# Kernel optimization log

Measured on AMD Instinct MI355X. Metric: run time of the kernel, lower is better.

Reference implementation:

```python
import jax, jax.numpy as jnp
import numpy as np

B, N, C, PH, PW = 16, 256, 1, 16, 16
G, HID = 8, 256
TEMP = 0.5
EPS = 1e-5


def setup_inputs() -> dict:
    key = jax.random.key(0)
    ks = jax.random.split(key, 16)
    f32 = jnp.float32
    def kaiming(k, shape):  # fan_out mode for convs, OIHW
        fan_out = shape[0] * shape[2] * shape[3]
        return jax.random.normal(k, shape, f32) * np.float32(np.sqrt(2.0 / fan_out))
    def lin(k, shape):  # nn.init.normal_(w, 0, 0.01)
        return jax.random.normal(k, shape, f32) * np.float32(0.01)
    return {
        "x": jax.random.normal(ks[0], (B, N, C, PH, PW), f32),
        "conv1_w": kaiming(ks[1], (32, 1, 3, 3)),  "conv1_b": jnp.zeros((32,), f32),
        "bn1_g": jnp.ones((32,), f32),  "bn1_b": jnp.zeros((32,), f32),
        "conv2_w": kaiming(ks[2], (64, 32, 3, 3)), "conv2_b": jnp.zeros((64,), f32),
        "bn2_g": jnp.ones((64,), f32),  "bn2_b": jnp.zeros((64,), f32),
        "conv3_w": kaiming(ks[3], (128, 64, 3, 3)), "conv3_b": jnp.zeros((128,), f32),
        "bn3_g": jnp.ones((128,), f32), "bn3_b": jnp.zeros((128,), f32),
        "fc_w": lin(ks[4], (HID, 128)),       "fc_b": jnp.zeros((HID,), f32),
        "g1_w": lin(ks[5], (2 * HID, HID)),   "g1_b": jnp.zeros((2 * HID,), f32),
        "ln1_g": jnp.ones((2 * HID,), f32),   "ln1_b": jnp.zeros((2 * HID,), f32),
        "g2_w": lin(ks[6], (2 * HID, 2 * HID)), "g2_b": jnp.zeros((2 * HID,), f32),
        "ln2_g": jnp.ones((2 * HID,), f32),   "ln2_b": jnp.zeros((2 * HID,), f32),
        "g3_w": lin(ks[7], (G, 2 * HID)),     "g3_b": jnp.zeros((G,), f32),
    }


def _conv(h, w, b):
    out = jax.lax.conv_general_dilated(h, w, (1, 1), 'SAME',
        dimension_numbers=('NCHW', 'OIHW', 'NCHW'))
    return out + b[None, :, None, None]


def _bn_train(h, g, b):  # batch stats over (N, H, W), biased variance
    m = h.mean(axis=(0, 2, 3), keepdims=True)
    v = h.var(axis=(0, 2, 3), keepdims=True)
    return (h - m) * jax.lax.rsqrt(v + EPS) * g[None, :, None, None] + b[None, :, None, None]


def _ln(h, g, b):
    m = h.mean(axis=-1, keepdims=True)
    v = h.var(axis=-1, keepdims=True)
    return (h - m) * jax.lax.rsqrt(v + EPS) * g + b


def reference(x, conv1_w, conv1_b, bn1_g, bn1_b, conv2_w, conv2_b, bn2_g, bn2_b,
              conv3_w, conv3_b, bn3_g, bn3_b, fc_w, fc_b,
              g1_w, g1_b, ln1_g, ln1_b, g2_w, g2_b, ln2_g, ln2_b, g3_w, g3_b):
    Bx, Nx, Cx, ph, pw = x.shape
    Gx = g3_w.shape[0]
    K = Nx // Gx  # num_patches_per_group

    # ---- patch encoder (conv + BN(train) + ReLU x3, GAP, Linear) ----
    h = x.reshape(Bx * Nx, Cx, ph, pw)
    h = jax.nn.relu(_bn_train(_conv(h, conv1_w, conv1_b), bn1_g, bn1_b))
    h = jax.nn.relu(_bn_train(_conv(h, conv2_w, conv2_b), bn2_g, bn2_b))
    h = jax.nn.relu(_bn_train(_conv(h, conv3_w, conv3_b), bn3_g, bn3_b))
    feat = h.mean(axis=(2, 3))                     # [B*N, 128] (AdaptiveAvgPool2d(1))
    feat = feat @ fc_w.T + fc_b                    # [B*N, HID]
    feat = feat.reshape(Bx, Nx, -1)

    # ---- grouping network ----
    h = jax.nn.relu(_ln(feat @ g1_w.T + g1_b, ln1_g, ln1_b))
    h = jax.nn.relu(_ln(h @ g2_w.T + g2_b, ln2_g, ln2_b))
    logits = (h @ g3_w.T + g3_b) / TEMP            # [B, N, G]
    assignment = jax.nn.softmax(logits, axis=2)    # [B, N, G]

    # ---- per-group top-K weighted patch gather (training path) ----
    w = jnp.transpose(assignment, (0, 2, 1))       # [B, G, N]
    vals, idx = jax.lax.top_k(w, K)                # [B, G, K] (descending, matches sort)
    idx_e = idx[:, :, :, None, None, None]         # [B, G, K, 1, 1, 1]
    gathered = jnp.take_along_axis(x[:, None], idx_e, axis=2)  # [B, G, K, C, ph, pw]
    output = gathered * vals[:, :, :, None, None, None]
    return output, assignment
```

## Files before the change

### kernel.cpp

```cpp
#include <hip/hip_runtime.h>


typedef float f32x16 __attribute__((ext_vector_type(16)));

#define WS_W1   0
#define WS_B1   288
#define WS_W2   320
#define WS_B2   18752
#define WS_W3   18816
#define WS_B3   92544
#define WS_FCW  92672
#define WS_FCB  125440
#define WS_G1W  125696
#define WS_G1B  256768
#define WS_L1G  257280
#define WS_L1B  257792
#define WS_G2W  258304
#define WS_G2B  520448
#define WS_L2G  520960
#define WS_L2B  521472
#define WS_G3W  521984
#define WS_G3B  526080
#define D_ACC1  263044
#define D_ACC2  (D_ACC1 + 4096)
#define D_ACC3  (D_ACC2 + 8192)
#define D_FEAT  (D_ACC3 + 16384)
#define D_AFF1  (D_FEAT + 524288)
#define D_AFF2  (D_AFF1 + 64)
#define D_AFF3  (D_AFF2 + 128)
#define D_ZN    553408
#define Z2_OFF_B 6532096ull


__global__ __launch_bounds__(256) void k_zero(double* __restrict__ dst){
  int i = blockIdx.x*256 + threadIdx.x;
  if(i < D_ZN) dst[i] = 0.0;
}

struct WP { const float* p[18]; };

__global__ __launch_bounds__(256) void k_cvt(WP wp, float* __restrict__ dst){
  const int segn[18] = {288,32,18432,64,73728,128,32768,256,131072,512,512,512,262144,512,512,512,4096,8};
  const int sego[18] = {WS_W1,WS_B1,WS_W2,WS_B2,WS_W3,WS_B3,WS_FCW,WS_FCB,WS_G1W,WS_G1B,
                        WS_L1G,WS_L1B,WS_G2W,WS_G2B,WS_L2G,WS_L2B,WS_G3W,WS_G3B};
  int s = blockIdx.y;
  int i = blockIdx.x*256 + threadIdx.x;
  if(i < segn[s]){
    if(s == 4){
      int oc = i / 576;
      int rem = i - oc*576;
      int ic = rem / 9;
      int j  = rem - ic*9;
      dst[WS_W3 + ic*1152 + j*128 + oc] = wp.p[4][i];
    } else {
      dst[sego[s]+i] = wp.p[s][i];
    }
  }
}

__global__ __launch_bounds__(64) void k_fin(const double* __restrict__ acc, int C,
                                            const float* __restrict__ gam, const float* __restrict__ bet,
                                            double* __restrict__ aff){
  int c = blockIdx.x, t = threadIdx.x;
  double s = acc[t*2*C + c*2];
  double q = acc[t*2*C + c*2 + 1];
  #pragma unroll
  for(int off=32;off;off>>=1){ s += __shfl_down(s,off); q += __shfl_down(q,off); }
  if(t==0){
    double m = s*(1.0/1048576.0);
    double v = q*(1.0/1048576.0) - m*m;
    double sc = (double)gam[c] / sqrt(v + 1e-5);
    aff[2*c]   = sc;
    aff[2*c+1] = (double)bet[c] - m*sc;
  }
}

__global__ __launch_bounds__(256) void k_p1(const float* __restrict__ x, const float* __restrict__ wf,
                                            double* __restrict__ acc1){
  __shared__ float xp[324];
  __shared__ double red[4][32][2];
  int p = blockIdx.x, t = threadIdx.x;
  for(int i=t;i<324;i+=256) xp[i]=0.f;
  __syncthreads();
  int py=t>>4, px=t&15;
  xp[(py+1)*18 + px + 1] = x[(size_t)p*256+t];
  __syncthreads();
  float nb[9];
  #pragma unroll
  for(int j=0;j<9;j++) nb[j] = xp[(py+j/3)*18 + px + (j%3)];
  int wave=t>>6, lane=t&63;
  for(int c=0;c<32;c++){
    float a = wf[WS_B1+c];
    #pragma unroll
    for(int j=0;j<9;j++) a = fmaf(nb[j], wf[WS_W1+c*9+j], a);
    double av=(double)a;
    double s=av, q=av*av;
    #pragma unroll
    for(int off=32;off;off>>=1){ s+=__shfl_down(s,off); q+=__shfl_down(q,off); }
    if(lane==0){ red[wave][c][0]=s; red[wave][c][1]=q; }
  }
  __syncthreads();
  if(t<64){
    int c=t>>1, st=t&1;
    double v = red[0][c][st]+red[1][c][st]+red[2][c][st]+red[3][c][st];
    atomicAdd(&acc1[(p&63)*64 + c*2 + st], v);
  }
}

__global__ __launch_bounds__(256) void k_p2(const float* __restrict__ x, const float* __restrict__ wf,
                                            const double* __restrict__ aff1, double* __restrict__ acc2,
                                            float* __restrict__ z2, int nS){
  __shared__ float xp[324];
  __shared__ float h1f[32*324];
  int p=blockIdx.x, t=threadIdx.x;
  for(int i=t;i<324;i+=256) xp[i]=0.f;
  for(int i=t;i<32*324;i+=256) h1f[i]=0.f;
  __syncthreads();
  int py=t>>4, px=t&15;
  xp[(py+1)*18 + px + 1] = x[(size_t)p*256+t];
  __syncthreads();
  {
    float nb[9];
    #pragma unroll
    for(int j=0;j<9;j++) nb[j] = xp[(py+j/3)*18 + px + (j%3)];
    for(int c=0;c<32;c++){
      float a = wf[WS_B1+c];
      #pragma unroll
      for(int j=0;j<9;j++) a = fmaf(nb[j], wf[WS_W1+c*9+j], a);
      h1f[c*324 + (py+1)*18 + (px+1)] = fmaxf(fmaf((float)aff1[2*c], a, (float)aff1[2*c+1]), 0.f);
    }
  }
  __syncthreads();
  int col=t&15, og=t>>4;
  bool wr = (p < nS);
  double sT[4]={0,0,0,0}, qT[4]={0,0,0,0};
  #pragma unroll 1
  for(int half=0; half<2; ++half){
    float acc[4][8];
    #pragma unroll
    for(int o=0;o<4;o++){
      float bv = wf[WS_B2 + og*4 + o];
      #pragma unroll
      for(int r=0;r<8;r++) acc[o][r]=bv;
    }
    #pragma unroll 1
    for(int ic=0; ic<32; ++ic){
      const float* wrow = wf + WS_W2 + (og*4*32 + ic)*9;
      #pragma unroll
      for(int j=0;j<9;j++){
        float w4[4];
        #pragma unroll
        for(int o=0;o<4;o++) w4[o] = wrow[o*288 + j];
        int dy=j/3, dx=j%3;
        #pragma unroll
        for(int r=0;r<8;r++){
          float m = h1f[ic*324 + (half*8 + r + dy)*18 + col + dx];
          #pragma unroll
          for(int o=0;o<4;o++) acc[o][r] = fmaf(m, w4[o], acc[o][r]);
        }
      }
    }
    #pragma unroll
    for(int o=0;o<4;o++){
      #pragma unroll
      for(int r=0;r<8;r++){ double v=(double)acc[o][r]; sT[o]+=v; qT[o]+=v*v; }
      if(wr){
        int c = og*4+o;
        #pragma unroll
        for(int r=0;r<8;r++) z2[((size_t)p*64+c)*256 + (half*8+r)*16 + col] = acc[o][r];
      }
    }
  }
  #pragma unroll
  for(int o=0;o<4;o++){
    double s=sT[o], q=qT[o];
    #pragma unroll
    for(int off=8;off;off>>=1){ s+=__shfl_down(s,off,16); q+=__shfl_down(q,off,16); }
    if(col==0){
      int c = og*4+o;
      atomicAdd(&acc2[(p&63)*128 + c*2 + 0], s);
      atomicAdd(&acc2[(p&63)*128 + c*2 + 1], q);
    }
  }
}

__global__ __launch_bounds__(512) void k_cs(const float* __restrict__ wf, const double* __restrict__ aff2,
                                            double* __restrict__ acc3, const float* __restrict__ z2){
  __shared__ float h2S[32*360];
  int p=blockIdx.x, t=threadIdx.x;
  for(int i=t;i<11520;i+=512) h2S[i]=0.f;
  int col=t&15, q=(t>>4)&3;
  int wv = __builtin_amdgcn_readfirstlane(t>>6);
  float acc[16][4];
  #pragma unroll
  for(int o=0;o<16;o++){
    float bv = wf[WS_B3 + wv*16 + o];
    #pragma unroll
    for(int r=0;r<4;r++) acc[o][r]=bv;
  }
  const f32x16* wW = reinterpret_cast<const f32x16*>(wf + WS_W3 + wv*16);
  #pragma unroll 1
  for(int half=0; half<2; ++half){
    __syncthreads();
    for(int i=t;i<8192;i+=512){
      int ch2 = i>>8, rem = i&255, gr = rem>>4, c2 = rem&15;
      int ch = half*32 + ch2;
      float zv = z2[((size_t)p*64+ch)*256 + gr*16 + c2];
      h2S[ch2*360 + (gr+1)*20 + c2+1] = fmaxf(fmaf((float)aff2[2*ch], zv, (float)aff2[2*ch+1]), 0.f);
    }
    __syncthreads();
    #pragma unroll 1
    for(int ic2=0; ic2<32; ++ic2){
      int ic = half*32 + ic2;
      float a[6][3];
      #pragma unroll
      for(int lr=0; lr<6; ++lr){
        #pragma unroll
        for(int dx=0; dx<3; ++dx) a[lr][dx] = h2S[ic2*360 + (4*q+lr)*20 + col + dx];
      }
      #pragma unroll
      for(int j=0;j<9;j++){
        f32x16 w = wW[ic*72 + j*8];
        int dy=j/3, dx=j%3;
        #pragma unroll
        for(int o=0;o<16;o++){
          #pragma unroll
          for(int r=0;r<4;r++) acc[o][r] = fmaf(a[r+dy][dx], w[o], acc[o][r]);
        }
      }
    }
  }
  #pragma unroll
  for(int o=0;o<16;o++){
    double s=0.0, q2=0.0;
    #pragma unroll
    for(int r=0;r<4;r++){ double v=(double)acc[o][r]; s+=v; q2+=v*v; }
    #pragma unroll
    for(int off=32;off;off>>=1){ s += __shfl_down(s,off); q2 += __shfl_down(q2,off); }
    if((t&63)==0){
      int c = wv*16+o;
      atomicAdd(&acc3[(p&63)*256 + c*2 + 0], s);
      atomicAdd(&acc3[(p&63)*256 + c*2 + 1], q2);
    }
  }
}

__global__ __launch_bounds__(512) void k_cf(const float* __restrict__ wf, const double* __restrict__ aff2,
                                            const double* __restrict__ aff3, double* __restrict__ feat,
                                            const float* __restrict__ z2){
  __shared__ float h2S[32*360];
  int p=blockIdx.x, t=threadIdx.x;
  for(int i=t;i<11520;i+=512) h2S[i]=0.f;
  int col=t&15, q=(t>>4)&3;
  int wv = __builtin_amdgcn_readfirstlane(t>>6);
  float acc[16][4];
  #pragma unroll
  for(int o=0;o<16;o++){
    float bv = wf[WS_B3 + wv*16 + o];
    #pragma unroll
    for(int r=0;r<4;r++) acc[o][r]=bv;
  }
  const f32x16* wW = reinterpret_cast<const f32x16*>(wf + WS_W3 + wv*16);
  #pragma unroll 1
  for(int half=0; half<2; ++half){
    __syncthreads();
    for(int i=t;i<8192;i+=512){
      int ch2 = i>>8, rem = i&255, gr = rem>>4, c2 = rem&15;
      int ch = half*32 + ch2;
      float zv = z2[((size_t)p*64+ch)*256 + gr*16 + c2];
      h2S[ch2*360 + (gr+1)*20 + c2+1] = fmaxf(fmaf((float)aff2[2*ch], zv, (float)aff2[2*ch+1]), 0.f);
    }
    __syncthreads();
    #pragma unroll 1
    for(int ic2=0; ic2<32; ++ic2){
      int ic = half*32 + ic2;
      float a[6][3];
      #pragma unroll
      for(int lr=0; lr<6; ++lr){
        #pragma unroll
        for(int dx=0; dx<3; ++dx) a[lr][dx] = h2S[ic2*360 + (4*q+lr)*20 + col + dx];
      }
      #pragma unroll
      for(int j=0;j<9;j++){
        f32x16 w = wW[ic*72 + j*8];
        int dy=j/3, dx=j%3;
        #pragma unroll
        for(int o=0;o<16;o++){
          #pragma unroll
          for(int r=0;r<4;r++) acc[o][r] = fmaf(a[r+dy][dx], w[o], acc[o][r]);
        }
      }
    }
  }
  #pragma unroll
  for(int o=0;o<16;o++){
    int c = wv*16+o;
    float sc=(float)aff3[2*c], sh=(float)aff3[2*c+1];
    double sv = 0.0;
    #pragma unroll
    for(int r=0;r<4;r++) sv += (double)fmaxf(fmaf(sc, acc[o][r], sh), 0.f);
    #pragma unroll
    for(int off=32;off;off>>=1) sv += __shfl_down(sv,off);
    if((t&63)==0) atomicAdd(&feat[(size_t)p*128 + c], sv);
  }
}

__global__ __launch_bounds__(256) void k_stat3(const float* __restrict__ x, const float* __restrict__ wf,
                                               const double* __restrict__ aff1, const double* __restrict__ aff2,
                                               double* __restrict__ acc3, int p0){
  __shared__ float xp[324];
  __shared__ float h1S[32*144];
  __shared__ float h2S[64*108];
  int bid=blockIdx.x, t=threadIdx.x;
  int p = p0 + (bid>>2), r0 = (bid&3)*4;
  for(int i=t;i<64*108;i+=256) h2S[i]=0.f;
  for(int i=t;i<324;i+=256) xp[i]=0.f;
  for(int i=t;i<32*144;i+=256) h1S[i]=0.f;
  __syncthreads();
  { int py=t>>4, px=t&15; xp[(py+1)*18 + px + 1] = x[(size_t)p*256+t]; }
  __syncthreads();
  {
    int rr=t>>5, cw=t&31, col=cw&15, half=cw>>4;
    int p1 = r0-1+rr;
    if(p1>=1 && p1<=16){
      float nb[9];
      #pragma unroll
      for(int j=0;j<9;j++) nb[j] = xp[(p1-1+j/3)*18 + col + (j%3)];
      for(int k=0;k<16;k++){
        int c = half*16+k;
        float a = wf[WS_B1+c];
        #pragma unroll
        for(int j=0;j<9;j++) a = fmaf(nb[j], wf[WS_W1+c*9+j], a);
        h1S[c*144 + rr*18 + col+1] = fmaxf((float)aff1[2*c]*a + (float)aff1[2*c+1], 0.f);
      }
    }
  }
  __syncthreads();
  {
    int col=t&15, g=t>>4;
    float a24[4][6];
    #pragma unroll
    for(int o=0;o<4;o++){
      float bv = wf[WS_B2+g*4+o];
      #pragma unroll
      for(int b2=0;b2<6;b2++) a24[o][b2] = bv;
    }
    #pragma unroll 1
    for(int ic=0;ic<32;ic++){
      const float* wrow = wf + WS_W2 + (g*4*32 + ic)*9;
      #pragma unroll
      for(int j=0;j<9;j++){
        float w4[4];
        #pragma unroll
        for(int o=0;o<4;o++) w4[o] = wrow[o*288 + j];
        int dy=j/3, dx=j%3;
        #pragma unroll
        for(int b2=0;b2<6;b2++){
          float m = h1S[ic*144 + (b2+dy)*18 + col + dx];
          #pragma unroll
          for(int o=0;o<4;o++) a24[o][b2] = fmaf(m, w4[o], a24[o][b2]);
        }
      }
    }
    #pragma unroll
    for(int b2=0;b2<6;b2++){
      int p2 = r0+b2;
      if(p2>=1 && p2<=16){
        #pragma unroll
        for(int o=0;o<4;o++){
          int c=g*4+o;
          h2S[c*108 + b2*18 + col+1] = fmaxf((float)aff2[2*c]*a24[o][b2] + (float)aff2[2*c+1], 0.f);
        }
      }
    }
  }
  __syncthreads();
  {
    int col = t & 15, og = t >> 4;
    float acc[8][4];
    #pragma unroll
    for(int o=0;o<8;o++){
      float bv = wf[WS_B3 + og*8 + o];
      #pragma unroll
      for(int r=0;r<4;r++) acc[o][r] = bv;
    }
    #pragma unroll 1
    for(int ic=0; ic<64; ++ic){
      float a[6][3];
      #pragma unroll
      for(int rr=0; rr<6; ++rr){
        #pragma unroll
        for(int dx=0; dx<3; ++dx) a[rr][dx] = h2S[ic*108 + rr*18 + col + dx];
      }
      const float* wrow = wf + WS_W3 + ic*1152;
      #pragma unroll
      for(int o=0;o<8;o++){
        #pragma unroll
        for(int j=0;j<9;j++){
          float w = wrow[j*128 + og*8 + o];
          #pragma unroll
          for(int r=0;r<4;r++) acc[o][r] = fmaf(a[r + j/3][j%3], w, acc[o][r]);
        }
      }
    }
    #pragma unroll
    for(int o=0;o<8;o++){
      double s=0.0, q=0.0;
      #pragma unroll
      for(int r=0;r<4;r++){ double v=(double)acc[o][r]; s+=v; q+=v*v; }
      #pragma unroll
      for(int off=8; off; off>>=1){ s += __shfl_down(s, off, 16); q += __shfl_down(q, off, 16); }
      if(col==0){
        int c = og*8+o;
        atomicAdd(&acc3[(bid&63)*256 + c*2 + 0], s);
        atomicAdd(&acc3[(bid&63)*256 + c*2 + 1], q);
      }
    }
  }
}

__global__ __launch_bounds__(256) void k_p34(const float* __restrict__ x, const float* __restrict__ wf,
                                             const double* __restrict__ aff1, const double* __restrict__ aff2,
                                             const double* __restrict__ aff3, double* __restrict__ outp,
                                             int p0){
  __shared__ float xp[324];
  __shared__ float h1S[32*144];
  __shared__ float h2S[64*108];
  int bid=blockIdx.x, t=threadIdx.x;
  int p = p0 + (bid>>2), r0 = (bid&3)*4;
  for(int i=t;i<64*108;i+=256) h2S[i]=0.f;
  for(int i=t;i<324;i+=256) xp[i]=0.f;
  for(int i=t;i<32*144;i+=256) h1S[i]=0.f;
  __syncthreads();
  { int py=t>>4, px=t&15; xp[(py+1)*18 + px + 1] = x[(size_t)p*256+t]; }
  __syncthreads();
  {
    int rr=t>>5, cw=t&31, col=cw&15, half=cw>>4;
    int p1 = r0-1+rr;
    if(p1>=1 && p1<=16){
      float nb[9];
      #pragma unroll
      for(int j=0;j<9;j++) nb[j] = xp[(p1-1+j/3)*18 + col + (j%3)];
      for(int k=0;k<16;k++){
        int c = half*16+k;
        float a = wf[WS_B1+c];
        #pragma unroll
        for(int j=0;j<9;j++) a = fmaf(nb[j], wf[WS_W1+c*9+j], a);
        h1S[c*144 + rr*18 + col+1] = fmaxf((float)aff1[2*c]*a + (float)aff1[2*c+1], 0.f);
      }
    }
  }
  __syncthreads();
  {
    int col=t&15, g=t>>4;
    float a24[4][6];
    #pragma unroll
    for(int o=0;o<4;o++){
      float bv = wf[WS_B2+g*4+o];
      #pragma unroll
      for(int b2=0;b2<6;b2++) a24[o][b2] = bv;
    }
    #pragma unroll 1
    for(int ic=0;ic<32;ic++){
      const float* wrow = wf + WS_W2 + (g*4*32 + ic)*9;
      #pragma unroll
      for(int j=0;j<9;j++){
        float w4[4];
        #pragma unroll
        for(int o=0;o<4;o++) w4[o] = wrow[o*288 + j];
        int dy=j/3, dx=j%3;
        #pragma unroll
        for(int b2=0;b2<6;b2++){
          float m = h1S[ic*144 + (b2+dy)*18 + col + dx];
          #pragma unroll
          for(int o=0;o<4;o++) a24[o][b2] = fmaf(m, w4[o], a24[o][b2]);
        }
      }
    }
    #pragma unroll
    for(int b2=0;b2<6;b2++){
      int p2 = r0+b2;
      if(p2>=1 && p2<=16){
        #pragma unroll
        for(int o=0;o<4;o++){
          int c=g*4+o;
          h2S[c*108 + b2*18 + col+1] = fmaxf((float)aff2[2*c]*a24[o][b2] + (float)aff2[2*c+1], 0.f);
        }
      }
    }
  }
  __syncthreads();
  {
    int col = t & 15, og = t >> 4;
    float acc[8][4];
    #pragma unroll
    for(int o=0;o<8;o++){
      float bv = wf[WS_B3 + og*8 + o];
      #pragma unroll
      for(int r=0;r<4;r++) acc[o][r] = bv;
    }
    #pragma unroll 1
    for(int ic=0; ic<64; ++ic){
      float a[6][3];
      #pragma unroll
      for(int rr=0; rr<6; ++rr){
        #pragma unroll
        for(int dx=0; dx<3; ++dx) a[rr][dx] = h2S[ic*108 + rr*18 + col + dx];
      }
      const float* wrow = wf + WS_W3 + ic*1152;
      #pragma unroll
      for(int o=0;o<8;o++){
        #pragma unroll
        for(int j=0;j<9;j++){
          float w = wrow[j*128 + og*8 + o];
          #pragma unroll
          for(int r=0;r<4;r++) acc[o][r] = fmaf(a[r + j/3][j%3], w, acc[o][r]);
        }
      }
    }
    #pragma unroll
    for(int o=0;o<8;o++){
      int c = og*8+o;
      float sc=(float)aff3[2*c], sh=(float)aff3[2*c+1];
      double s = 0.0;
      #pragma unroll
      for(int r=0;r<4;r++) s += (double)fmaxf(fmaf(sc, acc[o][r], sh), 0.f);
      #pragma unroll
      for(int off=8; off; off>>=1) s += __shfl_down(s, off, 16);
      if(col==0) atomicAdd(&outp[(size_t)p*128 + c], s);
    }
  }
}

__device__ __forceinline__ void ln_relu4(double* buf, const float* __restrict__ g, const float* __restrict__ b,
                                         double* lnm, double* lnr, int t){
  int r=t>>6, j=t&63;
  double s=0.0, q=0.0;
  for(int k=j;k<512;k+=64){ double v=buf[r*512+k]; s+=v; q+=v*v; }
  #pragma unroll
  for(int off=32;off;off>>=1){ s+=__shfl_down(s,off); q+=__shfl_down(q,off); }
  if(j==0){
    double m = s*(1.0/512.0);
    double v = q*(1.0/512.0) - m*m;
    lnm[r]=m; lnr[r]=1.0/sqrt(v + 1e-5);
  }
  __syncthreads();
  for(int i=t;i<2048;i+=256){
    int r2=i>>9, k=i&511;
    double v=(buf[i]-lnm[r2])*lnr[r2]*(double)g[k]+(double)b[k];
    buf[i]=fmax(v,0.0);
  }
  __syncthreads();
}

__global__ __launch_bounds__(256) void k_mlp(const float* __restrict__ wf, const double* __restrict__ feat,
                                             float* __restrict__ assign_out){
  int r0 = blockIdx.x*4, t = threadIdx.x;
  __shared__ double f0[4*128];
  __shared__ double f1[4*256];
  __shared__ double f2[4*512];
  __shared__ double f3[4*512];
  __shared__ double lnm[4], lnr[4];
  __shared__ double lg[4][8];

  for(int i=t;i<512;i+=256) f0[i] = feat[(size_t)r0*128 + i] * (1.0/256.0);
  __syncthreads();
  {
    double acc[4];
    double bv = (double)wf[WS_FCB + t];
    #pragma unroll
    for(int r=0;r<4;r++) acc[r]=bv;
    for(int k=0;k<128;k++){
      double wv = (double)wf[WS_FCW + t*128 + k];
      #pragma unroll
      for(int r=0;r<4;r++) acc[r]=fma(wv, f0[r*128+k], acc[r]);
    }
    #pragma unroll
    for(int r=0;r<4;r++) f1[r*256+t]=acc[r];
  }
  __syncthreads();
  for(int half=0;half<2;half++){
    int i=t+(half<<8);
    double acc[4];
    double bv=(double)wf[WS_G1B+i];
    #pragma unroll
    for(int r=0;r<4;r++) acc[r]=bv;
    for(int k=0;k<256;k++){
      double wv=(double)wf[WS_G1W + i*256 + k];
      #pragma unroll
      for(int r=0;r<4;r++) acc[r]=fma(wv, f1[r*256+k], acc[r]);
    }
    #pragma unroll
    for(int r=0;r<4;r++) f2[r*512+i]=acc[r];
  }
  __syncthreads();
  ln_relu4(f2, wf+WS_L1G, wf+WS_L1B, lnm, lnr, t);
  for(int half=0;half<2;half++){
    int i=t+(half<<8);
    double acc[4];
    double bv=(double)wf[WS_G2B+i];
    #pragma unroll
    for(int r=0;r<4;r++) acc[r]=bv;
    for(int k=0;k<512;k++){
      double wv=(double)wf[WS_G2W + i*512 + k];
      #pragma unroll
      for(int r=0;r<4;r++) acc[r]=fma(wv, f2[r*512+k], acc[r]);
    }
    #pragma unroll
    for(int r=0;r<4;r++) f3[r*512+i]=acc[r];
  }
  __syncthreads();
  ln_relu4(f3, wf+WS_L2G, wf+WS_L2B, lnm, lnr, t);
  {
    int r=t>>6, j=t&63;
    double pl[8];
    #pragma unroll
    for(int g=0;g<8;g++){
      double s=0.0;
      for(int k=j;k<512;k+=64) s = fma(f3[r*512+k], (double)wf[WS_G3W + g*512 + k], s);
      pl[g]=s;
    }
    #pragma unroll
    for(int off=32;off;off>>=1){
      #pragma unroll
      for(int g=0;g<8;g++) pl[g] += __shfl_down(pl[g], off);
    }
    if(j==0){
      #pragma unroll
      for(int g=0;g<8;g++) lg[r][g] = (pl[g] + (double)wf[WS_G3B+g]) * 2.0;
    }
  }
  __syncthreads();
  if(t<4){
    double m=-1e300;
    #pragma unroll
    for(int g=0;g<8;g++) m = fmax(m, lg[t][g]);
    double e[8], s=0.0;
    #pragma unroll
    for(int g=0;g<8;g++){ e[g]=exp(lg[t][g]-m); s+=e[g]; }
    double inv = 1.0/s;
    int row = r0 + t;
    #pragma unroll
    for(int g=0;g<8;g++) assign_out[row*8+g] = (float)(e[g]*inv);
  }
}

__global__ __launch_bounds__(256) void k_topk(const float* __restrict__ assign, const float* __restrict__ x,
                                              float* __restrict__ out){
  int b = blockIdx.x >> 3, g = blockIdx.x & 7, t = threadIdx.x;
  __shared__ float v[256];
  __shared__ int   id[256];
  v[t] = assign[(b*256+t)*8 + g];
  id[t] = t;
  __syncthreads();
  for(int k=2;k<=256;k<<=1){
    for(int j=k>>1;j>0;j>>=1){
      int ixj = t ^ j;
      if(ixj > t){
        float va=v[t], vb=v[ixj];
        int ia=id[t], ib=id[ixj];
        bool aBefore = (va > vb) || (va == vb && ia < ib);
        bool up = ((t & k) == 0);
        if(up != aBefore){ v[t]=vb; v[ixj]=va; id[t]=ib; id[ixj]=ia; }
      }
      __syncthreads();
    }
  }
  __shared__ float tv[32];
  __shared__ int   ti[32];
  if(t<32){ tv[t]=v[t]; ti[t]=id[t]; }
  __syncthreads();
  const float* xb = x + (size_t)b*65536;
  float* ob = out + (size_t)(b*8+g)*8192;
  for(int i=t;i<8192;i+=256){
    int k=i>>8, pix=i&255;
    ob[i] = tv[k] * xb[ti[k]*256 + pix];
  }
}

extern "C" void kernel_launch(void* const* d_in, const int* in_sizes, int n_in,
                              void* d_out, int out_size, void* d_ws, size_t ws_size,
                              hipStream_t stream){
  const float* x = (const float*)d_in[0];
  float*  ws  = (float*)d_ws;
  double* dws = (double*)d_ws;
  float* out = (float*)d_out;
  float* assign_out = out + 1048576;
  float* z2 = (float*)((char*)d_ws + Z2_OFF_B);

  int nS = 0;
  if(ws_size > Z2_OFF_B + 65536){
    unsigned long long avail = (unsigned long long)ws_size - Z2_OFF_B;
    unsigned long long n = avail / 65536ull;
    nS = (n > 4096ull) ? 4096 : (int)n;
  }
  int nR = 4096 - nS;

  const float* g1=(const float*)d_in[3];  const float* b1=(const float*)d_in[4];
  const float* g2=(const float*)d_in[7];  const float* b2=(const float*)d_in[8];
  const float* g3=(const float*)d_in[11]; const float* b3=(const float*)d_in[12];

  WP wp;
  const int map[18] = {1,2,5,6,9,10,13,14,15,16,17,18,19,20,21,22,23,24};
  for(int i=0;i<18;i++) wp.p[i] = (const float*)d_in[map[i]];

  k_zero <<<2162, 256, 0, stream>>>(dws + D_ACC1);
  k_cvt  <<<dim3(1024,18), 256, 0, stream>>>(wp, ws);
  k_p1   <<<4096, 256, 0, stream>>>(x, ws, dws+D_ACC1);
  k_fin  <<<32, 64, 0, stream>>>(dws+D_ACC1, 32, g1, b1, dws+D_AFF1);
  k_p2   <<<4096, 256, 0, stream>>>(x, ws, dws+D_AFF1, dws+D_ACC2, z2, nS);
  k_fin  <<<64, 64, 0, stream>>>(dws+D_ACC2, 64, g2, b2, dws+D_AFF2);
  if(nS > 0) k_cs   <<<nS, 512, 0, stream>>>(ws, dws+D_AFF2, dws+D_ACC3, z2);
  if(nR > 0) k_stat3<<<4*nR, 256, 0, stream>>>(x, ws, dws+D_AFF1, dws+D_AFF2, dws+D_ACC3, nS);
  k_fin  <<<128, 64, 0, stream>>>(dws+D_ACC3, 128, g3, b3, dws+D_AFF3);
  if(nS > 0) k_cf  <<<nS, 512, 0, stream>>>(ws, dws+D_AFF2, dws+D_AFF3, dws+D_FEAT, z2);
  if(nR > 0) k_p34 <<<4*nR, 256, 0, stream>>>(x, ws, dws+D_AFF1, dws+D_AFF2, dws+D_AFF3, dws+D_FEAT, nS);
  k_mlp  <<<1024, 256, 0, stream>>>(ws, dws+D_FEAT, assign_out);
  k_topk <<<128, 256, 0, stream>>>(assign_out, x, out);
}
```

Measured before the change: 4.066 ms.

## Use Winograd F(2,3) along columns for conv3 in k_cs and k_cf

Conv3 weights are pre-transformed into a 1D Winograd F(2,3) form along the width axis, stored in a new workspace region. The per-patch conv3 kernels then compute 2x2 output tiles per lane from transformed input rows, which cuts the FMAs per output and the LDS reads. The bias is now added after the inverse transform. This adds a prep segment to k_cvt and moves the z2 spill offset, and changes float rounding slightly.

```diff
diff --git a/kernel.cpp b/kernel.cpp
--- a/kernel.cpp
+++ b/kernel.cpp
@@ -29,7 +29,8 @@
 #define D_AFF2  (D_AFF1 + 64)
 #define D_AFF3  (D_AFF2 + 128)
 #define D_ZN    553408
-#define Z2_OFF_B 6532096ull
+#define W3T_F   1633024
+#define Z2_OFF_B 6925312ull
 
 
 __global__ __launch_bounds__(256) void k_zero(double* __restrict__ dst){
@@ -40,11 +41,22 @@
 struct WP { const float* p[18]; };
 
 __global__ __launch_bounds__(256) void k_cvt(WP wp, float* __restrict__ dst){
+  int s = blockIdx.y;
+  int i = blockIdx.x*256 + threadIdx.x;
+  if(s == 18){
+    if(i < 98304){
+      int ic = i/1536, r = i - ic*1536;
+      int ty = r>>9, r2 = r&511, k = r2>>7, oc = r2&127;
+      const float* src = wp.p[4] + ((size_t)oc*64 + ic)*9 + ty*3;
+      float w0=src[0], w1=src[1], w2=src[2];
+      float v = (k==0) ? w0 : (k==3) ? w2 : (k==1) ? (w0+w1+w2)*0.5f : (w0-w1+w2)*0.5f;
+      dst[W3T_F + i] = v;
+    }
+    return;
+  }
   const int segn[18] = {288,32,18432,64,73728,128,32768,256,131072,512,512,512,262144,512,512,512,4096,8};
   const int sego[18] = {WS_W1,WS_B1,WS_W2,WS_B2,WS_W3,WS_B3,WS_FCW,WS_FCB,WS_G1W,WS_G1B,
                         WS_L1G,WS_L1B,WS_G2W,WS_G2B,WS_L2G,WS_L2B,WS_G3W,WS_G3B};
-  int s = blockIdx.y;
-  int i = blockIdx.x*256 + threadIdx.x;
   if(i < segn[s]){
     if(s == 4){
       int oc = i / 576;
@@ -189,16 +201,18 @@
   __shared__ float h2S[32*360];
   int p=blockIdx.x, t=threadIdx.x;
   for(int i=t;i<11520;i+=512) h2S[i]=0.f;
-  int col=t&15, q=(t>>4)&3;
+  int l=t&63, cp=l&7, rg=l>>3;
   int wv = __builtin_amdgcn_readfirstlane(t>>6);
-  float acc[16][4];
+  float M[16][2][4];
   #pragma unroll
   for(int o=0;o<16;o++){
-    float bv = wf[WS_B3 + wv*16 + o];
-    #pragma unroll
-    for(int r=0;r<4;r++) acc[o][r]=bv;
-  }
-  const f32x16* wW = reinterpret_cast<const f32x16*>(wf + WS_W3 + wv*16);
+    #pragma unroll
+    for(int orr=0;orr<2;orr++){
+      #pragma unroll
+      for(int k=0;k<4;k++) M[o][orr][k]=0.f;
+    }
+  }
+  const f32x16* WT = reinterpret_cast<const f32x16*>(wf + W3T_F + wv*16);
   #pragma unroll 1
   for(int half=0; half<2; ++half){
     __syncthreads();
@@ -212,29 +226,44 @@
     #pragma unroll 1
     for(int ic2=0; ic2<32; ++ic2){
       int ic = half*32 + ic2;
-      float a[6][3];
-      #pragma unroll
-      for(int lr=0; lr<6; ++lr){
-        #pragma unroll
-        for(int dx=0; dx<3; ++dx) a[lr][dx] = h2S[ic2*360 + (4*q+lr)*20 + col + dx];
-      }
-      #pragma unroll
-      for(int j=0;j<9;j++){
-        f32x16 w = wW[ic*72 + j*8];
-        int dy=j/3, dx=j%3;
+      float vt[4][4];
+      #pragma unroll
+      for(int lr=0; lr<4; ++lr){
+        float d0 = h2S[ic2*360 + (2*rg+lr)*20 + 2*cp + 0];
+        float d1 = h2S[ic2*360 + (2*rg+lr)*20 + 2*cp + 1];
+        float d2 = h2S[ic2*360 + (2*rg+lr)*20 + 2*cp + 2];
+        float d3 = h2S[ic2*360 + (2*rg+lr)*20 + 2*cp + 3];
+        vt[lr][0]=d0-d2; vt[lr][1]=d1+d2; vt[lr][2]=d2-d1; vt[lr][3]=d1-d3;
+      }
+      #pragma unroll
+      for(int ty=0;ty<3;ty++){
+        f32x16 w0 = WT[(size_t)((ic*3+ty)*4+0)*8];
+        f32x16 w1 = WT[(size_t)((ic*3+ty)*4+1)*8];
+        f32x16 w2 = WT[(size_t)((ic*3+ty)*4+2)*8];
+        f32x16 w3 = WT[(size_t)((ic*3+ty)*4+3)*8];
         #pragma unroll
         for(int o=0;o<16;o++){
           #pragma unroll
-          for(int r=0;r<4;r++) acc[o][r] = fmaf(a[r+dy][dx], w[o], acc[o][r]);
+          for(int orr=0;orr<2;orr++){
+            M[o][orr][0] = fmaf(vt[orr+ty][0], w0[o], M[o][orr][0]);
+            M[o][orr][1] = fmaf(vt[orr+ty][1], w1[o], M[o][orr][1]);
+            M[o][orr][2] = fmaf(vt[orr+ty][2], w2[o], M[o][orr][2]);
+            M[o][orr][3] = fmaf(vt[orr+ty][3], w3[o], M[o][orr][3]);
+          }
         }
       }
     }
   }
   #pragma unroll
   for(int o=0;o<16;o++){
-    double s=0.0, q2=0.0;
-    #pragma unroll
-    for(int r=0;r<4;r++){ double v=(double)acc[o][r]; s+=v; q2+=v*v; }
+    float bv = wf[WS_B3 + wv*16 + o];
+    float y00 = M[o][0][0]+M[o][0][1]+M[o][0][2] + bv;
+    float y01 = M[o][0][1]-M[o][0][2]-M[o][0][3] + bv;
+    float y10 = M[o][1][0]+M[o][1][1]+M[o][1][2] + bv;
+    float y11 = M[o][1][1]-M[o][1][2]-M[o][1][3] + bv;
+    double s  = (double)y00+(double)y01+(double)y10+(double)y11;
+    double q2 = (double)y00*(double)y00+(double)y01*(double)y01
+              + (double)y10*(double)y10+(double)y11*(double)y11;
     #pragma unroll
     for(int off=32;off;off>>=1){ s += __shfl_down(s,off); q2 += __shfl_down(q2,off); }
     if((t&63)==0){
@@ -251,16 +280,18 @@
   __shared__ float h2S[32*360];
   int p=blockIdx.x, t=threadIdx.x;
   for(int i=t;i<11520;i+=512) h2S[i]=0.f;
-  int col=t&15, q=(t>>4)&3;
+  int l=t&63, cp=l&7, rg=l>>3;
   int wv = __builtin_amdgcn_readfirstlane(t>>6);
-  float acc[16][4];
+  float M[16][2][4];
   #pragma unroll
   for(int o=0;o<16;o++){
-    float bv = wf[WS_B3 + wv*16 + o];
-    #pragma unroll
-    for(int r=0;r<4;r++) acc[o][r]=bv;
-  }
-  const f32x16* wW = reinterpret_cast<const f32x16*>(wf + WS_W3 + wv*16);
+    #pragma unroll
+    for(int orr=0;orr<2;orr++){
+      #pragma unroll
+      for(int k=0;k<4;k++) M[o][orr][k]=0.f;
+    }
+  }
+  const f32x16* WT = reinterpret_cast<const f32x16*>(wf + W3T_F + wv*16);
   #pragma unroll 1
   for(int half=0; half<2; ++half){
     __syncthreads();
@@ -274,20 +305,30 @@
     #pragma unroll 1
     for(int ic2=0; ic2<32; ++ic2){
       int ic = half*32 + ic2;
-      float a[6][3];
-      #pragma unroll
-      for(int lr=0; lr<6; ++lr){
-        #pragma unroll
-        for(int dx=0; dx<3; ++dx) a[lr][dx] = h2S[ic2*360 + (4*q+lr)*20 + col + dx];
-      }
-      #pragma unroll
-      for(int j=0;j<9;j++){
-        f32x16 w = wW[ic*72 + j*8];
-        int dy=j/3, dx=j%3;
+      float vt[4][4];
+      #pragma unroll
+      for(int lr=0; lr<4; ++lr){
+        float d0 = h2S[ic2*360 + (2*rg+lr)*20 + 2*cp + 0];
+        float d1 = h2S[ic2*360 + (2*rg+lr)*20 + 2*cp + 1];
+        float d2 = h2S[ic2*360 + (2*rg+lr)*20 + 2*cp + 2];
+        float d3 = h2S[ic2*360 + (2*rg+lr)*20 + 2*cp + 3];
+        vt[lr][0]=d0-d2; vt[lr][1]=d1+d2; vt[lr][2]=d2-d1; vt[lr][3]=d1-d3;
+      }
+      #pragma unroll
+      for(int ty=0;ty<3;ty++){
+        f32x16 w0 = WT[(size_t)((ic*3+ty)*4+0)*8];
+        f32x16 w1 = WT[(size_t)((ic*3+ty)*4+1)*8];
+        f32x16 w2 = WT[(size_t)((ic*3+ty)*4+2)*8];
+        f32x16 w3 = WT[(size_t)((ic*3+ty)*4+3)*8];
         #pragma unroll
         for(int o=0;o<16;o++){
           #pragma unroll
-          for(int r=0;r<4;r++) acc[o][r] = fmaf(a[r+dy][dx], w[o], acc[o][r]);
+          for(int orr=0;orr<2;orr++){
+            M[o][orr][0] = fmaf(vt[orr+ty][0], w0[o], M[o][orr][0]);
+            M[o][orr][1] = fmaf(vt[orr+ty][1], w1[o], M[o][orr][1]);
+            M[o][orr][2] = fmaf(vt[orr+ty][2], w2[o], M[o][orr][2]);
+            M[o][orr][3] = fmaf(vt[orr+ty][3], w3[o], M[o][orr][3]);
+          }
         }
       }
     }
@@ -295,10 +336,16 @@
   #pragma unroll
   for(int o=0;o<16;o++){
     int c = wv*16+o;
+    float bv = wf[WS_B3 + c];
     float sc=(float)aff3[2*c], sh=(float)aff3[2*c+1];
-    double sv = 0.0;
-    #pragma unroll
-    for(int r=0;r<4;r++) sv += (double)fmaxf(fmaf(sc, acc[o][r], sh), 0.f);
+    float y00 = M[o][0][0]+M[o][0][1]+M[o][0][2] + bv;
+    float y01 = M[o][0][1]-M[o][0][2]-M[o][0][3] + bv;
+    float y10 = M[o][1][0]+M[o][1][1]+M[o][1][2] + bv;
+    float y11 = M[o][1][1]-M[o][1][2]-M[o][1][3] + bv;
+    double sv = (double)fmaxf(fmaf(sc, y00, sh), 0.f)
+              + (double)fmaxf(fmaf(sc, y01, sh), 0.f)
+              + (double)fmaxf(fmaf(sc, y10, sh), 0.f)
+              + (double)fmaxf(fmaf(sc, y11, sh), 0.f);
     #pragma unroll
     for(int off=32;off;off>>=1) sv += __shfl_down(sv,off);
     if((t&63)==0) atomicAdd(&feat[(size_t)p*128 + c], sv);
@@ -705,7 +752,7 @@
   for(int i=0;i<18;i++) wp.p[i] = (const float*)d_in[map[i]];
 
   k_zero <<<2162, 256, 0, stream>>>(dws + D_ACC1);
-  k_cvt  <<<dim3(1024,18), 256, 0, stream>>>(wp, ws);
+  k_cvt  <<<dim3(1024,19), 256, 0, stream>>>(wp, ws);
   k_p1   <<<4096, 256, 0, stream>>>(x, ws, dws+D_ACC1);
   k_fin  <<<32, 64, 0, stream>>>(dws+D_ACC1, 32, g1, b1, dws+D_AFF1);
   k_p2   <<<4096, 256, 0, stream>>>(x, ws, dws+D_AFF1, dws+D_ACC2, z2, nS);
```

Measured after the change: 5.538 ms. +36.2%, slower.
